# Kernel tuning notes

Measured on AMD Instinct MI355X. Metric: run time of the kernel, lower is better.

## Reference

```python
import jax, jax.numpy as jnp
import numpy as np

KH, KW = 3, 3
STRIDE = (1, 1)
PAD = (1, 1)
DIL = (1, 1)
DG = 1  # num_deformable_groups


def _out_size(h, pad, dil, k, stride):
    return (h + 2 * pad - (dil * (k - 1) + 1)) // stride + 1


def setup_inputs() -> dict:
    key = jax.random.key(0)
    k1, k2, k3 = jax.random.split(key, 3)
    B, Cin, H, W = 8, 128, 64, 64
    Cout = 128
    Ho = _out_size(H, PAD[0], DIL[0], KH, STRIDE[0])
    Wo = _out_size(W, PAD[1], DIL[1], KW, STRIDE[1])
    x = jax.random.normal(k1, (B, Cin, H, W), jnp.float32)
    offset = jax.random.normal(k2, (B, 2 * DG * KH * KW, Ho, Wo), jnp.float32)
    n = Cin * KH * KW
    stdv = 1.0 / np.sqrt(n)
    weight = jax.random.uniform(k3, (Cout, Cin, KH, KW), jnp.float32, -stdv, stdv)
    return {"x": x, "offset": offset, "weight": weight}


def deform_conv2d(x, offset, weight):
    B, Cin, H, W = x.shape
    Cout, _, kh, kw = weight.shape
    K = kh * kw
    Ho = _out_size(H, PAD[0], DIL[0], kh, STRIDE[0])
    Wo = _out_size(W, PAD[1], DIL[1], kw, STRIDE[1])
    G = DG
    Cg = Cin // G

    # base sampling grid per kernel tap: [kh,kw,Ho,Wo]
    by = (jnp.arange(kh) * DIL[0])[:, None, None, None] + (jnp.arange(Ho) * STRIDE[0] - PAD[0])[None, None, :, None]
    bx = (jnp.arange(kw) * DIL[1])[None, :, None, None] + (jnp.arange(Wo) * STRIDE[1] - PAD[1])[None, None, None, :]
    by = jnp.broadcast_to(by, (kh, kw, Ho, Wo)).reshape(K, Ho, Wo).astype(x.dtype)
    bx = jnp.broadcast_to(bx, (kh, kw, Ho, Wo)).reshape(K, Ho, Wo).astype(x.dtype)

    # offset layout: channel = g*2*K + 2*k + {0: dy, 1: dx}
    off = offset.reshape(B, G, K, 2, Ho, Wo)
    py = by[None, None] + off[:, :, :, 0]  # [B,G,K,Ho,Wo]
    px = bx[None, None] + off[:, :, :, 1]

    y0 = jnp.floor(py).astype(jnp.int32)
    x0 = jnp.floor(px).astype(jnp.int32)
    wy = (py - y0).reshape(B, G, 1, -1)  # fractional parts, [B,G,1,K*Ho*Wo]
    wx = (px - x0).reshape(B, G, 1, -1)

    xg = x.reshape(B, G, Cg, H * W)
    N = K * Ho * Wo

    def gather(yi, xi):
        valid = ((yi >= 0) & (yi < H) & (xi >= 0) & (xi < W)).reshape(B, G, 1, N)
        idx = (jnp.clip(yi, 0, H - 1) * W + jnp.clip(xi, 0, W - 1)).reshape(B, G, 1, N)
        v = jnp.take_along_axis(xg, jnp.broadcast_to(idx, (B, G, Cg, N)), axis=3)
        return v * valid.astype(x.dtype)

    v00 = gather(y0, x0)
    v01 = gather(y0, x0 + 1)
    v10 = gather(y0 + 1, x0)
    v11 = gather(y0 + 1, x0 + 1)

    cols = (v00 * (1 - wy) * (1 - wx) + v01 * (1 - wy) * wx
            + v10 * wy * (1 - wx) + v11 * wy * wx)
    cols = cols.reshape(B, G, Cg, K, Ho, Wo)  # deformable im2col columns

    wr = weight.reshape(Cout, G, Cg, K)
    return jnp.einsum('ogck,bgcknm->bonm', wr, cols)


def reference(x, offset, weight):
    return deform_conv2d(x, offset, weight)
```

## Files before the change

kernel.cpp:

```cpp
#include <hip/hip_runtime.h>
#include <hip/hip_fp16.h>

typedef __attribute__((ext_vector_type(4))) float f32x4;
typedef __attribute__((ext_vector_type(8))) _Float16 f16x8;
typedef __attribute__((ext_vector_type(4))) unsigned int u32x4;

__device__ __forceinline__ unsigned short f2h(float f) {
  __half h = __float2half_rn(f);
  unsigned short u;
  __builtin_memcpy(&u, &h, 2);
  return u;
}
__device__ __forceinline__ __half2 h2_of(unsigned int u) {
  __half2 h;
  __builtin_memcpy(&h, &u, 4);
  return h;
}
__device__ __forceinline__ unsigned int u_of(__half2 h) {
  unsigned int u;
  __builtin_memcpy(&u, &h, 4);
  return u;
}

__global__ __launch_bounds__(256) void prep_kernel(const float* __restrict__ x,
                                                   const float* __restrict__ w,
                                                   unsigned short* __restrict__ xt,
                                                   unsigned short* __restrict__ wf) {
  if (blockIdx.x < 2048) {
    int t = blockIdx.x * 256 + threadIdx.x;
    int p  = t & 4095;
    int cg = (t >> 12) & 15;
    int b  = t >> 16;
    const float* xp = x + (((size_t)(b * 128 + cg * 8)) << 12) + p;
    unsigned int r[8];
#pragma unroll
    for (int j = 0; j < 8; ++j) r[j] = f2h(xp[(size_t)j << 12]);
    u32x4 pk;
    pk.x = r[0] | (r[1] << 16);
    pk.y = r[2] | (r[3] << 16);
    pk.z = r[4] | (r[5] << 16);
    pk.w = r[6] | (r[7] << 16);
    *reinterpret_cast<u32x4*>(xt + ((((size_t)b << 12) + p) << 7) + cg * 8) = pk;
  } else {
    int tid = (blockIdx.x - 2048) * 256 + threadIdx.x;
    int l  = tid & 63;
    int mt = (tid >> 6) & 7;
    int ch = tid >> 9;
    int cc = ch / 9, tap = ch - cc * 9;
    int co = mt * 16 + (l & 15);
    int cb = cc * 32 + (l >> 4) * 8;
    unsigned int r[8];
#pragma unroll
    for (int j = 0; j < 8; ++j)
      r[j] = f2h(w[(co * 128 + cb + j) * 9 + tap]);
    u32x4 pk;
    pk.x = r[0] | (r[1] << 16);
    pk.y = r[2] | (r[3] << 16);
    pk.z = r[4] | (r[5] << 16);
    pk.w = r[6] | (r[7] << 16);
    *reinterpret_cast<u32x4*>(wf + (size_t)tid * 8) = pk;
  }
}

__global__ __launch_bounds__(512, 1) void deform_kernel(const unsigned short* __restrict__ xt,
                                                        const float* __restrict__ off,
                                                        const unsigned short* __restrict__ wf,
                                                        float* __restrict__ out) {
  __shared__ __align__(16) unsigned char sWin[137216];
  __shared__ int   sPos[1152];
  __shared__ uint2 sWt[1152];

  const int tid = threadIdx.x;
  const int bid = blockIdx.x;
  const int b   = bid & 7;
  const int ho0 = (bid >> 3) * 2;
  const int r0  = min(max(ho0 - 3, 0), 56);

  {
    const unsigned short* xrow = xt + ((size_t)b << 19) + ((size_t)r0 << 13);
#pragma unroll
    for (int it = 0; it < 16; ++it) {
      int idx = it * 512 + tid;
      int c = idx & 15;
      int p = (idx >> 4) & 63;
      int r = idx >> 10;
      u32x4 v;
      __builtin_memcpy(&v, xrow + (((size_t)(r * 64 + p)) << 7) + c * 8, 16);
      *reinterpret_cast<u32x4*>(&sWin[r * 16384 + p * 256 + (((c + p) & 15) << 4)]) = v;
    }
  }

  for (int r = tid; r < 1152; r += 512) {
    int row = (r >= 576) ? 1 : 0;
    int rr  = r - row * 576;
    int tap = rr >> 6, wo = rr & 63;
    int ho = ho0 + row;
    float dy = off[((b * 18 + 2 * tap)     * 64 + ho) * 64 + wo];
    float dx = off[((b * 18 + 2 * tap + 1) * 64 + ho) * 64 + wo];
    float py = (float)(ho + (tap / 3) - 1) + dy;
    float px = (float)(wo + (tap % 3) - 1) + dx;
    float fy = floorf(py), fx = floorf(px);
    int y0 = (int)fy, x0 = (int)fx;
    float wy = py - fy, wx = px - fx;
    float wt = (y0 >= 0 && y0 < 64) ? (1.f - wy) : 0.f;
    float wb = (y0 + 1 >= 0 && y0 + 1 < 64) ? wy : 0.f;
    int y0c = min(max(y0, 0), 63), y1c = min(max(y0 + 1, 0), 63);
    int bx; float wl, wr;
    if (x0 >= 0 && x0 <= 62)      { bx = x0; wl = 1.f - wx; wr = wx;       }
    else if (x0 == -1)            { bx = 0;  wl = wx;       wr = 0.f;      }
    else if (x0 == 63)            { bx = 62; wl = 0.f;      wr = 1.f - wx; }
    else                          { bx = 0;  wl = 0.f;      wr = 0.f;      }
    sPos[r] = (y0c * 64 + bx) | ((y1c != y0c) ? (1 << 15) : 0);
    __half2 tp = __floats2half2_rn(wt * wl, wt * wr);
    __half2 bp = __floats2half2_rn(wb * wl, wb * wr);
    uint2 ww;
    ww.x = u_of(tp);
    ww.y = u_of(bp);
    sWt[r] = ww;
  }
  __syncthreads();

  const int l   = tid & 63;
  const int w   = tid >> 6;
  const int ks  = w & 3;
  const int row = w >> 2;
  const int ln  = l & 15;
  const int kg  = l >> 4;
  const int c16 = ks * 4 + kg;
  const int ho  = ho0 + row;

  const unsigned short* xtb = xt + ((size_t)b << 19) + ks * 32 + kg * 8;
  const unsigned short* wfb = wf + (size_t)l * 8;

  f32x4 acc[4][8] = {};

  for (int tap = 0; tap < 9; ++tap) {
    const int ch = ks * 9 + tap;

    f16x8 A[8];
    const unsigned short* wp = wfb + (size_t)(ch * 8) * 512;
#pragma unroll
    for (int mt = 0; mt < 8; ++mt)
      A[mt] = *reinterpret_cast<const f16x8*>(wp + (size_t)mt * 512);

#pragma unroll
    for (int pg = 0; pg < 4; ++pg) {
      const int e = row * 576 + tap * 64 + pg * 16 + ln;
      const int   pp = sPos[e];
      const uint2 ww = sWt[e];

      const int aX = pp & 4095;
      const int aY = aX + ((pp >> 9) & 64);
      const int tx  = aX & 63;
      const int twr = (aX >> 6) - r0;
      const int bwr = (aY >> 6) - r0;
      const bool tin = (unsigned)twr < 8u;
      const bool bin = (unsigned)bwr < 8u;

      u32x4 T0, T1, B0, B1;
      {
        int cT0 = ((c16 + tx) & 15) << 4, cT1 = ((c16 + tx + 1) & 15) << 4;
        int baseT = (tin ? twr : 0) * 16384 + tx * 256;
        __builtin_memcpy(&T0, &sWin[baseT + cT0],       16);
        __builtin_memcpy(&T1, &sWin[baseT + 256 + cT1], 16);
        int baseB = (bin ? bwr : 0) * 16384 + tx * 256;
        __builtin_memcpy(&B0, &sWin[baseB + cT0],       16);
        __builtin_memcpy(&B1, &sWin[baseB + 256 + cT1], 16);
      }
      if (!tin) {
        const unsigned short* p0 = xtb + ((size_t)aX << 7);
        __builtin_memcpy(&T0, p0,       16);
        __builtin_memcpy(&T1, p0 + 128, 16);
      }
      if (!bin) {
        const unsigned short* p1 = xtb + ((size_t)aY << 7);
        __builtin_memcpy(&B0, p1,       16);
        __builtin_memcpy(&B1, p1 + 128, 16);
      }

      const __half2 wtl = __half2half2(__low2half(h2_of(ww.x)));
      const __half2 wtr = __half2half2(__high2half(h2_of(ww.x)));
      const __half2 wbl = __half2half2(__low2half(h2_of(ww.y)));
      const __half2 wbr = __half2half2(__high2half(h2_of(ww.y)));
      u32x4 pk;
#pragma unroll
      for (int d = 0; d < 4; ++d) {
        __half2 s = __hmul2(wtl, h2_of(T0[d]));
        s = __hfma2(wtr, h2_of(T1[d]), s);
        s = __hfma2(wbl, h2_of(B0[d]), s);
        s = __hfma2(wbr, h2_of(B1[d]), s);
        pk[d] = u_of(s);
      }
      f16x8 bfrag;
      __builtin_memcpy(&bfrag, &pk, 16);

#pragma unroll
      for (int mt = 0; mt < 8; ++mt)
        acc[pg][mt] = __builtin_amdgcn_mfma_f32_16x16x32_f16(A[mt], bfrag,
                                                             acc[pg][mt], 0, 0, 0);
    }
  }

  float* sF = reinterpret_cast<float*>(sWin);
#define WR_LDS(BASE)                                                           \
  { _Pragma("unroll") for (int pg = 0; pg < 4; ++pg)                           \
    _Pragma("unroll") for (int mt = 0; mt < 8; ++mt)                           \
      *reinterpret_cast<f32x4*>(&sF[(BASE) + row * 8448 + (pg * 16 + ln) * 132 + mt * 16 + kg * 4]) = acc[pg][mt]; }
#define RD_LDS(BASE)                                                           \
  { _Pragma("unroll") for (int pg = 0; pg < 4; ++pg)                           \
    _Pragma("unroll") for (int mt = 0; mt < 8; ++mt) {                         \
      f32x4 v = *reinterpret_cast<const f32x4*>(&sF[(BASE) + row * 8448 + (pg * 16 + ln) * 132 + mt * 16 + kg * 4]); \
      acc[pg][mt] += v; } }

  __syncthreads();
  if (ks == 1) WR_LDS(17408)
  if (ks == 3) WR_LDS(0)
  __syncthreads();
  if (ks == 0) RD_LDS(17408)
  if (ks == 2) RD_LDS(0)
  __syncthreads();
  if (ks == 2) WR_LDS(17408)
  __syncthreads();
  if (ks == 0) RD_LDS(17408)
#undef WR_LDS
#undef RD_LDS

  {
    const int b2 = row * 8704;
    if (ks == 0) {
#pragma unroll
      for (int pg = 0; pg < 4; ++pg)
#pragma unroll
        for (int mt = 0; mt < 8; ++mt)
#pragma unroll
          for (int rg = 0; rg < 4; ++rg)
            sF[b2 + (mt * 16 + kg * 4 + rg) * 68 + pg * 16 + ln] = acc[pg][mt][rg];
    }
    __syncthreads();
    if (ks == 0) {
      const int q4  = l & 15;
      const int ch2 = l >> 4;
      float* ob = out + (((size_t)b * 128) * 64 + ho) * 64 + q4 * 4;
#pragma unroll
      for (int i = 0; i < 32; ++i) {
        int co = ch2 * 32 + i;
        f32x4 v = *reinterpret_cast<const f32x4*>(&sF[b2 + co * 68 + q4 * 4]);
        *reinterpret_cast<f32x4*>(ob + (size_t)co * 4096) = v;
      }
    }
  }
}

extern "C" void kernel_launch(void* const* d_in, const int* in_sizes, int n_in,
                              void* d_out, int out_size, void* d_ws, size_t ws_size,
                              hipStream_t stream) {
  (void)in_sizes; (void)n_in; (void)out_size; (void)ws_size;
  const float* x   = (const float*)d_in[0];
  const float* off = (const float*)d_in[1];
  const float* w   = (const float*)d_in[2];
  float* out = (float*)d_out;
  unsigned short* xt = (unsigned short*)d_ws;
  unsigned short* wf = (unsigned short*)d_ws + (8388608 / 2);

  prep_kernel<<<2120, 256, 0, stream>>>(x, w, xt, wf);
  deform_kernel<<<256, 512, 0, stream>>>(xt, off, wf, out);
}
```

Baseline: 100.8 us.

## Pad LDS window rows instead of XOR swizzle and batch gathers before MFMAs

Replaces the rotating channel swizzle in the shared-memory input window with a padded row stride of 272 bytes per pixel, which simplifies the address arithmetic. Splits the per-tap loop so that all four pixel groups' LDS and global corner loads are issued before any interpolation or MFMA work, letting memory latency overlap. The padding grows shared memory use slightly, may change the bank-conflict pattern, and holding 16 vectors per tap raises register pressure.

Result: no change. 99.99 us (-0.8%).

```diff
diff --git a/kernel.cpp b/kernel.cpp
--- a/kernel.cpp
+++ b/kernel.cpp
@@ -66,7 +66,7 @@
                                                         const float* __restrict__ off,
                                                         const unsigned short* __restrict__ wf,
                                                         float* __restrict__ out) {
-  __shared__ __align__(16) unsigned char sWin[137216];
+  __shared__ __align__(16) unsigned char sWin[8 * 17408];
   __shared__ int   sPos[1152];
   __shared__ uint2 sWt[1152];
 
@@ -86,7 +86,7 @@
       int r = idx >> 10;
       u32x4 v;
       __builtin_memcpy(&v, xrow + (((size_t)(r * 64 + p)) << 7) + c * 8, 16);
-      *reinterpret_cast<u32x4*>(&sWin[r * 16384 + p * 256 + (((c + p) & 15) << 4)]) = v;
+      *reinterpret_cast<u32x4*>(&sWin[r * 17408 + p * 272 + c * 16]) = v;
     }
   }
 
@@ -126,7 +126,7 @@
   const int row = w >> 2;
   const int ln  = l & 15;
   const int kg  = l >> 4;
-  const int c16 = ks * 4 + kg;
+  const int koff = ks * 64 + kg * 16;
   const int ho  = ho0 + row;
 
   const unsigned short* xtb = xt + ((size_t)b << 19) + ks * 32 + kg * 8;
@@ -143,11 +143,13 @@
     for (int mt = 0; mt < 8; ++mt)
       A[mt] = *reinterpret_cast<const f16x8*>(wp + (size_t)mt * 512);
 
+    u32x4 T0[4], T1[4], B0[4], B1[4];
+    uint2 wws[4];
 #pragma unroll
     for (int pg = 0; pg < 4; ++pg) {
       const int e = row * 576 + tap * 64 + pg * 16 + ln;
-      const int   pp = sPos[e];
-      const uint2 ww = sWt[e];
+      const int pp = sPos[e];
+      wws[pg] = sWt[e];
 
       const int aX = pp & 4095;
       const int aY = aX + ((pp >> 9) & 64);
@@ -157,27 +159,28 @@
       const bool tin = (unsigned)twr < 8u;
       const bool bin = (unsigned)bwr < 8u;
 
-      u32x4 T0, T1, B0, B1;
-      {
-        int cT0 = ((c16 + tx) & 15) << 4, cT1 = ((c16 + tx + 1) & 15) << 4;
-        int baseT = (tin ? twr : 0) * 16384 + tx * 256;
-        __builtin_memcpy(&T0, &sWin[baseT + cT0],       16);
-        __builtin_memcpy(&T1, &sWin[baseT + 256 + cT1], 16);
-        int baseB = (bin ? bwr : 0) * 16384 + tx * 256;
-        __builtin_memcpy(&B0, &sWin[baseB + cT0],       16);
-        __builtin_memcpy(&B1, &sWin[baseB + 256 + cT1], 16);
-      }
+      const int laT = (tin ? twr : 0) * 17408 + tx * 272 + koff;
+      __builtin_memcpy(&T0[pg], &sWin[laT],       16);
+      __builtin_memcpy(&T1[pg], &sWin[laT + 272], 16);
+      const int laB = (bin ? bwr : 0) * 17408 + tx * 272 + koff;
+      __builtin_memcpy(&B0[pg], &sWin[laB],       16);
+      __builtin_memcpy(&B1[pg], &sWin[laB + 272], 16);
+
       if (!tin) {
         const unsigned short* p0 = xtb + ((size_t)aX << 7);
-        __builtin_memcpy(&T0, p0,       16);
-        __builtin_memcpy(&T1, p0 + 128, 16);
+        __builtin_memcpy(&T0[pg], p0,       16);
+        __builtin_memcpy(&T1[pg], p0 + 128, 16);
       }
       if (!bin) {
         const unsigned short* p1 = xtb + ((size_t)aY << 7);
-        __builtin_memcpy(&B0, p1,       16);
-        __builtin_memcpy(&B1, p1 + 128, 16);
-      }
-
+        __builtin_memcpy(&B0[pg], p1,       16);
+        __builtin_memcpy(&B1[pg], p1 + 128, 16);
+      }
+    }
+
+#pragma unroll
+    for (int pg = 0; pg < 4; ++pg) {
+      const uint2 ww = wws[pg];
       const __half2 wtl = __half2half2(__low2half(h2_of(ww.x)));
       const __half2 wtr = __half2half2(__high2half(h2_of(ww.x)));
       const __half2 wbl = __half2half2(__low2half(h2_of(ww.y)));
@@ -185,10 +188,10 @@
       u32x4 pk;
 #pragma unroll
       for (int d = 0; d < 4; ++d) {
-        __half2 s = __hmul2(wtl, h2_of(T0[d]));
-        s = __hfma2(wtr, h2_of(T1[d]), s);
-        s = __hfma2(wbl, h2_of(B0[d]), s);
-        s = __hfma2(wbr, h2_of(B1[d]), s);
+        __half2 s = __hmul2(wtl, h2_of(T0[pg][d]));
+        s = __hfma2(wtr, h2_of(T1[pg][d]), s);
+        s = __hfma2(wbl, h2_of(B0[pg][d]), s);
+        s = __hfma2(wbr, h2_of(B1[pg][d]), s);
         pk[d] = u_of(s);
       }
       f16x8 bfrag;
```
